# Kernel optimization log

Hardware: AMD Instinct MI355X
Metric: run time of the kernel (lower is better)

The kernel has to match this reference:

```python
import jax, jax.numpy as jnp
import numpy as np

N = 100000
E = 1000000
D = 32          # numerical_dim
HID = 64        # hidden_dim
OUT = 1         # output_dim
REL = 4 * D     # relation feature dim
EPS = 1e-8


def setup_inputs() -> dict:
    key = jax.random.key(0)
    k_x, k_e, k_w1, k_b1, k_w2, k_b2 = jax.random.split(key, 6)
    x = jax.random.uniform(k_x, (N, D), dtype=jnp.float32)
    edge_index = jax.random.randint(k_e, (2, E), 0, N, dtype=jnp.int64)
    # Linear params (PyTorch convention: W [out, in], y = x @ W.T + b)
    lim1 = 1.0 / np.sqrt(REL)
    W1 = jax.random.uniform(k_w1, (HID, REL), minval=-lim1, maxval=lim1, dtype=jnp.float32)
    b1 = jax.random.uniform(k_b1, (HID,), minval=-lim1, maxval=lim1, dtype=jnp.float32)
    lim2 = 1.0 / np.sqrt(HID)
    W2 = jax.random.uniform(k_w2, (OUT, HID), minval=-lim2, maxval=lim2, dtype=jnp.float32)
    b2 = jax.random.uniform(k_b2, (OUT,), minval=-lim2, maxval=lim2, dtype=jnp.float32)
    return {"x": x, "edge_index": edge_index, "W1": W1, "b1": b1, "W2": W2, "b2": b2}


def _relation_features(x_i, x_j):
    ratio = x_i / (x_j + EPS)
    log_ratio = jnp.log(x_i + EPS) - jnp.log(x_j + EPS)
    abs_diff = jnp.abs(x_i - x_j)
    rel_diff = abs_diff / (jnp.maximum(x_i, x_j) + EPS)
    return jnp.concatenate([ratio, log_ratio, abs_diff, rel_diff], axis=-1)  # [E, 4D]


def reference(x, edge_index, W1, b1, W2, b2):
    src, dst = edge_index[0], edge_index[1]
    x_i = x[src]                      # [E, D] gather source node feats
    x_j = x[dst]                      # [E, D] gather target node feats
    rel = _relation_features(x_i, x_j)  # [E, 4D]
    h = jax.nn.relu(rel @ W1.T + b1)    # [E, HID]
    edge_bias = (h @ W2.T + b2).squeeze(-1)  # [E]
    return edge_bias
```

## Files before the change

### kernel.cpp

```cpp
#include <hip/hip_runtime.h>


#define DD    32
#define HID   64
#define RELF  128
#define EPSF  1e-8f
#define LXLO  -18.420681f
#define LXSC  13.843137f
#define LXIV  0.07223796f
#define MSC   3.0517578125e-05f

typedef short  bf16x8 __attribute__((ext_vector_type(8)));
typedef float  f32x16 __attribute__((ext_vector_type(16)));

union U8 { unsigned u[4]; bf16x8 v; uint4 q4; };
union Q  { uint4 v; unsigned u[4]; float f[4]; };

static __device__ __forceinline__ unsigned pk_tr(float lo, float hi) {
    return __builtin_amdgcn_perm(__builtin_bit_cast(unsigned, hi),
                                 __builtin_bit_cast(unsigned, lo), 0x07060302u);
}
static __device__ __forceinline__ unsigned rne_bits(float f) {
    unsigned u = __builtin_bit_cast(unsigned, f);
    return u + 0x7fffu + ((u >> 16) & 1u);
}
static __device__ __forceinline__ unsigned pk_rne(float lo, float hi) {
    return __builtin_amdgcn_perm(rne_bits(hi), rne_bits(lo), 0x07060302u);
}
static __device__ __forceinline__ float hi_f32(float f) {
    return __builtin_bit_cast(float, __builtin_bit_cast(unsigned, f) & 0xffff0000u);
}
static __device__ __forceinline__ float ubyte(unsigned w, int b) {
    return (float)((w >> (8 * b)) & 0xffu);
}
static __device__ __forceinline__ unsigned q8(float v) {
    int u = (int)(v + 0.5f);
    return (unsigned)(u > 255 ? 255 : (u < 0 ? 0 : u));
}
template <int CTRL>
static __device__ __forceinline__ float dpp_ror_add(float pp) {
    int s = __builtin_bit_cast(int, pp);
    int t = __builtin_amdgcn_update_dpp(0, s, CTRL, 0xf, 0xf, true);
    return pp + __builtin_bit_cast(float, t);
}

__global__ __launch_bounds__(256)
void prep_pack(const float* __restrict__ x, uint4* __restrict__ rec, int nchunk)
{
    int i = blockIdx.x * blockDim.x + threadIdx.x;
    if (i >= nchunk) return;
    const float4* xp = (const float4*)(x + (size_t)i * 8);
    float4 v0 = xp[0], v1 = xp[1];
    float xv[8] = {v0.x, v0.y, v0.z, v0.w, v1.x, v1.y, v1.z, v1.w};

    unsigned xh[4];
    #pragma unroll
    for (int p = 0; p < 4; ++p) xh[p] = pk_tr(xv[2*p], xv[2*p+1]);

    unsigned xl[2] = {0u, 0u}, lu[2] = {0u, 0u};
    #pragma unroll
    for (int e = 0; e < 8; ++e) {
        float a  = xv[e];
        float ah = hi_f32(a);
        float f  = 0.f;
        if (ah > 0.f)
            f = (a * __builtin_amdgcn_rcpf(ah) - 1.f) * 32768.f;
        xl[e >> 2] |= q8(f) << (8 * (e & 3));
        float lxe = __logf(a + EPSF);
        lu[e >> 2] |= q8((lxe - LXLO) * LXSC) << (8 * (e & 3));
    }

    uint4 r0; r0.x = xh[0]; r0.y = xh[1]; r0.z = xh[2]; r0.w = xh[3];
    uint4 r1; r1.x = xl[0]; r1.y = xl[1]; r1.z = lu[0]; r1.w = lu[1];
    rec[2 * i]     = r0;
    rec[2 * i + 1] = r1;
}

template <int PACK>
__global__ __launch_bounds__(256, 3)
void edge_bias_mfma(const float* __restrict__ x,
                    const int*   __restrict__ ei,
                    const float* __restrict__ W1,
                    const float* __restrict__ b1,
                    const float* __restrict__ W2,
                    const float* __restrict__ b2,
                    const uint4* __restrict__ rec,
                    float* __restrict__ out,
                    int E)
{
    const int lane = threadIdx.x & 63;
    const int wv   = threadIdx.x >> 6;
    const int wave = (blockIdx.x * blockDim.x + threadIdx.x) >> 6;
    const int nwv  = (gridDim.x * blockDim.x) >> 6;
    const int r = lane & 31;
    const int h = lane >> 5;

    __shared__ uint4 sW[20 * 64];
    for (int f = wv; f < 20; f += 4) {
        const int set = f >> 2, ct = (f >> 1) & 1, sl = f & 1;
        const int fb  = (set <= 1) ? 0 : (set - 1) * 32;
        const float* wr = W1 + (ct * 32 + r) * RELF + fb + sl * 16 + h * 8;
        U8 tw;
        if (set == 0) {
            #pragma unroll
            for (int p = 0; p < 4; ++p) tw.u[p] = pk_tr(wr[2*p], wr[2*p+1]);
        } else if (set == 1) {
            #pragma unroll
            for (int p = 0; p < 4; ++p) {
                float w0 = wr[2*p], w1 = wr[2*p+1];
                tw.u[p] = pk_rne(w0 - hi_f32(w0), w1 - hi_f32(w1));
            }
        } else {
            #pragma unroll
            for (int p = 0; p < 4; ++p) tw.u[p] = pk_rne(wr[2*p], wr[2*p+1]);
        }
        sW[f * 64 + lane] = tw.q4;
    }
    __syncthreads();

    float b1v[2], w2v[2];
    #pragma unroll
    for (int ct = 0; ct < 2; ++ct) {
        b1v[ct] = b1[ct * 32 + r];
        w2v[ct] = W2[ct * 32 + r];
    }
    const float b2s = b2[0];

    auto decode = [&](const Q& hq, const Q& mq, float* xv, bf16x8& lfrag) {
        #pragma unroll
        for (int p = 0; p < 4; ++p) {
            float lo = __builtin_bit_cast(float, hq.u[p] << 16);
            float hi = __builtin_bit_cast(float, hq.u[p] & 0xffff0000u);
            unsigned xb = (p < 2) ? mq.u[0] : mq.u[1];
            float m0 = ubyte(xb, (2 * p) & 3);
            float m1 = ubyte(xb, (2 * p + 1) & 3);
            xv[2 * p]     = fmaf(lo * MSC, m0, lo);
            xv[2 * p + 1] = fmaf(hi * MSC, m1, hi);
        }
        U8 L;
        #pragma unroll
        for (int p = 0; p < 4; ++p) {
            unsigned lb = (p < 2) ? mq.u[2] : mq.u[3];
            float l0 = fmaf(ubyte(lb, (2 * p) & 3),     LXIV, LXLO);
            float l1 = fmaf(ubyte(lb, (2 * p + 1) & 3), LXIV, LXLO);
            L.u[p] = pk_tr(l0, l1);
        }
        lfrag = L.v;
    };

    const int ntiles = (E + 31) >> 5;
    for (int t = wave; t < ntiles; t += nwv) {
        int em = (t << 5) + r; if (em > E - 1) em = E - 1;
        const int sn = ei[em], dn = ei[E + em];

        Q hi0, mi0, hi1, mi1, hj0, mj0, hj1, mj1;
        if constexpr (PACK) {
            const uint4* pi = rec + (size_t)sn * 8 + (h << 1);
            const uint4* pj = rec + (size_t)dn * 8 + (h << 1);
            hi0.v = pi[0]; mi0.v = pi[1]; hi1.v = pi[4]; mi1.v = pi[5];
            hj0.v = pj[0]; mj0.v = pj[1]; hj1.v = pj[4]; mj1.v = pj[5];
        } else {
            const uint4* pi = (const uint4*)(x + (size_t)sn * DD + h * 8);
            const uint4* pj = (const uint4*)(x + (size_t)dn * DD + h * 8);
            hi0.v = pi[0]; mi0.v = pi[1]; hi1.v = pi[4]; mi1.v = pi[5];
            hj0.v = pj[0]; mj0.v = pj[1]; hj1.v = pj[4]; mj1.v = pj[5];
        }

        int off = lane;
        asm volatile("" : "+v"(off));
        auto ldfrag = [&](int set, int ct, int sl) {
            U8 w; w.q4 = sW[(set * 4 + ct * 2 + sl) * 64 + off];
            return w.v;
        };

        f32x16 acc0, acc1;
        #pragma unroll
        for (int i = 0; i < 16; ++i) { acc0[i] = b1v[0]; acc1[i] = b1v[1]; }

        #pragma unroll
        for (int sl = 0; sl < 2; ++sl) {
            const Q& hI = sl ? hi1 : hi0;  const Q& mI = sl ? mi1 : mi0;
            const Q& hJ = sl ? hj1 : hj0;  const Q& mJ = sl ? mj1 : mj0;

            float xiv[8], xjv[8];
            bf16x8 aLi, aLj;
            if constexpr (PACK) {
                decode(hI, mI, xiv, aLi);
                decode(hJ, mJ, xjv, aLj);
            } else {
                #pragma unroll
                for (int p = 0; p < 4; ++p) {
                    xiv[p] = hI.f[p]; xiv[4 + p] = mI.f[p];
                    xjv[p] = hJ.f[p]; xjv[4 + p] = mJ.f[p];
                }
                U8 ti, tj;
                #pragma unroll
                for (int p = 0; p < 4; ++p) {
                    ti.u[p] = pk_rne(__logf(xiv[2*p] + EPSF), __logf(xiv[2*p+1] + EPSF));
                    tj.u[p] = pk_rne(__logf(xjv[2*p] + EPSF), __logf(xjv[2*p+1] + EPSF));
                }
                aLi = ti.v; aLj = tj.v;
            }
            U8 nj; nj.v = aLj;
            #pragma unroll
            for (int p = 0; p < 4; ++p) nj.u[p] ^= 0x80008000u;

            U8 R, Rl, Aa, Dd;
            #pragma unroll
            for (int p = 0; p < 4; ++p) {
                float a0 = xiv[2*p], a1 = xiv[2*p+1];
                float c0 = xjv[2*p], c1 = xjv[2*p+1];
                float r0 = a0 * __builtin_amdgcn_rcpf(c0 + EPSF);
                float r1 = a1 * __builtin_amdgcn_rcpf(c1 + EPSF);
                float d0 = fabsf(a0 - c0), d1 = fabsf(a1 - c1);
                float g0 = d0 * __builtin_amdgcn_rcpf(fmaxf(a0, c0) + EPSF);
                float g1 = d1 * __builtin_amdgcn_rcpf(fmaxf(a1, c1) + EPSF);
                R.u[p]  = pk_tr(r0, r1);
                Rl.u[p] = pk_tr(r0 - hi_f32(r0), r1 - hi_f32(r1));
                Aa.u[p] = pk_tr(d0, d1);
                Dd.u[p] = pk_tr(g0, g1);
            }

            #pragma unroll
            for (int ct = 0; ct < 2; ++ct) {
                bf16x8 fW0h = ldfrag(0, ct, sl);
                bf16x8 fW0l = ldfrag(1, ct, sl);
                bf16x8 fWL  = ldfrag(2, ct, sl);
                bf16x8 fWA  = ldfrag(3, ct, sl);
                bf16x8 fWD  = ldfrag(4, ct, sl);
                if (ct == 0) {
                    acc0 = __builtin_amdgcn_mfma_f32_32x32x16_bf16(R.v,  fW0h, acc0, 0, 0, 0);
                    acc0 = __builtin_amdgcn_mfma_f32_32x32x16_bf16(Rl.v, fW0h, acc0, 0, 0, 0);
                    acc0 = __builtin_amdgcn_mfma_f32_32x32x16_bf16(R.v,  fW0l, acc0, 0, 0, 0);
                    acc0 = __builtin_amdgcn_mfma_f32_32x32x16_bf16(aLi,  fWL,  acc0, 0, 0, 0);
                    acc0 = __builtin_amdgcn_mfma_f32_32x32x16_bf16(nj.v, fWL,  acc0, 0, 0, 0);
                    acc0 = __builtin_amdgcn_mfma_f32_32x32x16_bf16(Aa.v, fWA,  acc0, 0, 0, 0);
                    acc0 = __builtin_amdgcn_mfma_f32_32x32x16_bf16(Dd.v, fWD,  acc0, 0, 0, 0);
                } else {
                    acc1 = __builtin_amdgcn_mfma_f32_32x32x16_bf16(R.v,  fW0h, acc1, 0, 0, 0);
                    acc1 = __builtin_amdgcn_mfma_f32_32x32x16_bf16(Rl.v, fW0h, acc1, 0, 0, 0);
                    acc1 = __builtin_amdgcn_mfma_f32_32x32x16_bf16(R.v,  fW0l, acc1, 0, 0, 0);
                    acc1 = __builtin_amdgcn_mfma_f32_32x32x16_bf16(aLi,  fWL,  acc1, 0, 0, 0);
                    acc1 = __builtin_amdgcn_mfma_f32_32x32x16_bf16(nj.v, fWL,  acc1, 0, 0, 0);
                    acc1 = __builtin_amdgcn_mfma_f32_32x32x16_bf16(Aa.v, fWA,  acc1, 0, 0, 0);
                    acc1 = __builtin_amdgcn_mfma_f32_32x32x16_bf16(Dd.v, fWD,  acc1, 0, 0, 0);
                }
            }
        }

        #pragma unroll
        for (int g = 0; g < 16; ++g) {
            float s = fmaf(fmaxf(acc0[g], 0.f), w2v[0],
                           fmaxf(acc1[g], 0.f) * w2v[1]);
            s = dpp_ror_add<0x121>(s);
            s = dpp_ror_add<0x122>(s);
            s = dpp_ror_add<0x124>(s);
            s = dpp_ror_add<0x128>(s);
            s = dpp_ror_add<0x142>(s);
            if ((((lane >> 4) & 1) != 0) && (lane & 15) == g) {
                const int e2 = (t << 5) + (g & 3) + ((g >> 2) << 3) + (h << 2);
                if (e2 < E) out[e2] = s + b2s;
            }
        }
    }
}

extern "C" void kernel_launch(void* const* d_in, const int* in_sizes, int n_in,
                              void* d_out, int out_size, void* d_ws, size_t ws_size,
                              hipStream_t stream)
{
    const float* x   = (const float*)d_in[0];
    const int*   ei  = (const int*)  d_in[1];
    const float* W1  = (const float*)d_in[2];
    const float* b1  = (const float*)d_in[3];
    const float* W2  = (const float*)d_in[4];
    const float* b2  = (const float*)d_in[5];
    float* out = (float*)d_out;

    const int E  = out_size;
    const int Nd = in_sizes[0];
    uint4* rec = (uint4*)d_ws;

    const int blocks = 1954;

    const bool pack = ws_size >= (size_t)Nd * 4 && (Nd % 8) == 0;
    if (pack) {
        const int nchunk = Nd / 8;
        prep_pack<<<(nchunk + 255) / 256, 256, 0, stream>>>(x, rec, nchunk);
        edge_bias_mfma<1><<<blocks, 256, 0, stream>>>(x, ei, W1, b1, W2, b2, rec, out, E);
    } else {
        edge_bias_mfma<0><<<blocks, 256, 0, stream>>>(x, ei, W1, b1, W2, b2, rec, out, E);
    }
}
```

Baseline: 138.9 us.

## Software-pipeline edge index loads and node gathers two tiles ahead

Restructures the per-wave tile loop into a double-buffered pipeline. Node-feature gathers for the next tile sit in a second register set, and edge indices are prefetched three tiles ahead, so global-memory latency overlaps with the MFMA compute of the current tile. The cost is more VGPRs for the extra gather buffers, which may lower occupancy, plus redundant loads of a clamped tile near the end.

```diff
diff --git a/kernel.cpp b/kernel.cpp
--- a/kernel.cpp
+++ b/kernel.cpp
@@ -149,23 +149,31 @@
     };
 
     const int ntiles = (E + 31) >> 5;
-    for (int t = wave; t < ntiles; t += nwv) {
-        int em = (t << 5) + r; if (em > E - 1) em = E - 1;
-        const int sn = ei[em], dn = ei[E + em];
-
-        Q hi0, mi0, hi1, mi1, hj0, mj0, hj1, mj1;
+    int t = wave;
+    if (t >= ntiles) return;
+
+    auto ldidx = [&](int tt, int& s, int& d) {
+        if (tt >= ntiles) tt = t;
+        int em = (tt << 5) + r; if (em > E - 1) em = E - 1;
+        s = ei[em]; d = ei[E + em];
+    };
+    auto gather = [&](int sn, int dn, Q& h0, Q& m0, Q& h1, Q& m1,
+                                      Q& g0, Q& n0, Q& g1, Q& n1) {
         if constexpr (PACK) {
             const uint4* pi = rec + (size_t)sn * 8 + (h << 1);
             const uint4* pj = rec + (size_t)dn * 8 + (h << 1);
-            hi0.v = pi[0]; mi0.v = pi[1]; hi1.v = pi[4]; mi1.v = pi[5];
-            hj0.v = pj[0]; mj0.v = pj[1]; hj1.v = pj[4]; mj1.v = pj[5];
+            h0.v = pi[0]; m0.v = pi[1]; h1.v = pi[4]; m1.v = pi[5];
+            g0.v = pj[0]; n0.v = pj[1]; g1.v = pj[4]; n1.v = pj[5];
         } else {
             const uint4* pi = (const uint4*)(x + (size_t)sn * DD + h * 8);
             const uint4* pj = (const uint4*)(x + (size_t)dn * DD + h * 8);
-            hi0.v = pi[0]; mi0.v = pi[1]; hi1.v = pi[4]; mi1.v = pi[5];
-            hj0.v = pj[0]; mj0.v = pj[1]; hj1.v = pj[4]; mj1.v = pj[5];
-        }
-
+            h0.v = pi[0]; m0.v = pi[1]; h1.v = pi[4]; m1.v = pi[5];
+            g0.v = pj[0]; n0.v = pj[1]; g1.v = pj[4]; n1.v = pj[5];
+        }
+    };
+
+    auto compute = [&](int tc, const Q& hi0, const Q& mi0, const Q& hi1, const Q& mi1,
+                               const Q& hj0, const Q& mj0, const Q& hj1, const Q& mj1) {
         int off = lane;
         asm volatile("" : "+v"(off));
         auto ldfrag = [&](int set, int ct, int sl) {
@@ -258,10 +266,30 @@
             s = dpp_ror_add<0x128>(s);
             s = dpp_ror_add<0x142>(s);
             if ((((lane >> 4) & 1) != 0) && (lane & 15) == g) {
-                const int e2 = (t << 5) + (g & 3) + ((g >> 2) << 3) + (h << 2);
+                const int e2 = (tc << 5) + (g & 3) + ((g >> 2) << 3) + (h << 2);
                 if (e2 < E) out[e2] = s + b2s;
             }
         }
+    };
+
+    Q hiA0, miA0, hiA1, miA1, hjA0, mjA0, hjA1, mjA1;
+    Q hiB0, miB0, hiB1, miB1, hjB0, mjB0, hjB1, mjB1;
+    int sC, dC;
+
+    { int s, d; ldidx(t,       s, d); gather(s, d, hiA0, miA0, hiA1, miA1, hjA0, mjA0, hjA1, mjA1); }
+    { int s, d; ldidx(t + nwv, s, d); gather(s, d, hiB0, miB0, hiB1, miB1, hjB0, mjB0, hjB1, mjB1); }
+    ldidx(t + 2 * nwv, sC, dC);
+
+    for (;;) {
+        compute(t, hiA0, miA0, hiA1, miA1, hjA0, mjA0, hjA1, mjA1);
+        gather(sC, dC, hiA0, miA0, hiA1, miA1, hjA0, mjA0, hjA1, mjA1);
+        ldidx(t + 3 * nwv, sC, dC);
+        t += nwv; if (t >= ntiles) break;
+
+        compute(t, hiB0, miB0, hiB1, miB1, hjB0, mjB0, hjB1, mjB1);
+        gather(sC, dC, hiB0, miB0, hiB1, miB1, hjB0, mjB0, hjB1, mjB1);
+        ldidx(t + 3 * nwv, sC, dC);
+        t += nwv; if (t >= ntiles) break;
     }
 }
 
```

After: 146.9 us. 1.06x slower.
